# Performance work log

Hardware: AMD Instinct MI355X
Metric: run time of the kernel (lower is better)

## Reference

```python
import jax, jax.numpy as jnp
import numpy as np
from jax import lax

NB, NL, ND, NF = 32, 1024, 128, 16   # batch, max_nodes, d_model, n_func_groups
DT_RANK, NS, DCONV = 8, 2, 4         # ceil(128/16), d_state, d_conv


def setup_inputs() -> dict:
    key = jax.random.key(0)
    ks = jax.random.split(key, 16)
    s = 0.05
    x = jax.random.normal(ks[0], (NB, NL, ND), jnp.float32)
    # dense distance-weighted adjacency; scale by 1/NL so delta_p = dis @ delta stays O(1)
    dis_dense = jax.random.uniform(ks[1], (NB, NL, NL), dtype=jnp.float32) / NL
    gpt_emb = jax.random.normal(ks[2], (NB, ND), jnp.float32)
    fg_emb = jax.random.normal(ks[3], (NB, NF, ND), jnp.float32)
    A_log = jnp.log(jnp.tile(jnp.arange(1, NS + 1, dtype=jnp.float32), (ND, 1)))  # [d, n]
    return {
        "x": x, "dis_dense": dis_dense, "gpt_emb": gpt_emb, "fg_emb": fg_emb,
        "norm_w": jnp.ones((ND,), jnp.float32),
        "in_proj_w": jax.random.normal(ks[4], (2 * ND, ND), jnp.float32) * s,
        "conv_w": jax.random.normal(ks[5], (ND, 1, DCONV), jnp.float32) * s,  # depthwise OIH
        "conv_b": jax.random.normal(ks[6], (ND,), jnp.float32) * s,
        "x_proj_w": jax.random.normal(ks[7], (DT_RANK + 2 * NS, ND), jnp.float32) * s,
        "dt_proj_w": jax.random.normal(ks[8], (ND, DT_RANK), jnp.float32) * s,
        "dt_proj_b": jax.random.normal(ks[9], (ND,), jnp.float32) * s,
        "A_log": A_log,
        "D_skip": jnp.ones((ND,), jnp.float32),
        "out_proj_w": jax.random.normal(ks[10], (ND, ND), jnp.float32) * s,
        "film_w1": jax.random.normal(ks[11], (ND, ND), jnp.float32) * s,
        "film_b1": jax.random.normal(ks[12], (ND,), jnp.float32) * s,
        "film_w2": jax.random.normal(ks[13], (2 * ND, ND), jnp.float32) * s,
        "film_b2": jax.random.normal(ks[14], (2 * ND,), jnp.float32) * s,
    }


def reference(x, dis_dense, gpt_emb, fg_emb, norm_w, in_proj_w, conv_w, conv_b,
              x_proj_w, dt_proj_w, dt_proj_b, A_log, D_skip, out_proj_w,
              film_w1, film_b1, film_w2, film_b2):
    d_model = x.shape[-1]
    # RMSNorm
    x1 = x * lax.rsqrt(jnp.mean(x * x, axis=-1, keepdims=True) + 1e-5) * norm_w
    atoms = x1  # gnn treated as identity
    # CrossAttentionFusion: Q=atoms, K=V=fg_emb
    attn = jax.nn.softmax(jnp.einsum('bnd,bfd->bnf', atoms, fg_emb)
                          / jnp.sqrt(jnp.asarray(d_model, x.dtype)), axis=-1)
    h = atoms + jnp.einsum('bnf,bfd->bnd', attn, fg_emb)
    # FiLM conditioning from gpt_emb
    gb = jax.nn.silu(gpt_emb @ film_w1.T + film_b1) @ film_w2.T + film_b2
    gamma, beta = jnp.split(gb, 2, axis=-1)
    h = h * gamma[:, None, :] + beta[:, None, :]
    # in_proj -> (x, res)
    xr = h @ in_proj_w.T
    xin, res = jnp.split(xr, 2, axis=-1)
    # depthwise causal conv1d (pad d_conv-1 on the left, truncate to l)
    xc = lax.conv_general_dilated(xin.transpose(0, 2, 1), conv_w, (1,), [(DCONV - 1, 0)],
                                  dimension_numbers=('NCH', 'OIH', 'NCH'),
                                  feature_group_count=d_model) + conv_b[None, :, None]
    xs = jax.nn.silu(xc.transpose(0, 2, 1))  # [b, l, d]
    # SSM parameterization
    x_dbl = xs @ x_proj_w.T
    dt, Bm, Cm = jnp.split(x_dbl, [DT_RANK, DT_RANK + NS], axis=-1)
    delta = jax.nn.softplus(dt @ dt_proj_w.T + dt_proj_b)  # [b, l, d]
    A = -jnp.exp(A_log)  # [d, n]
    # graph-mixed delta
    delta_p = jnp.einsum('blm,bmd->bld', dis_dense, delta)
    dA = jnp.exp(jnp.einsum('bld,dn->bldn', delta_p, A))
    dBu = jnp.einsum('bld,bln,bld->bldn', delta_p, Bm, xs)
    # sequential selective scan over l
    def step(state, inp):
        a, bu, c = inp                      # [b,d,n], [b,d,n], [b,n]
        state = a * state + bu
        return state, jnp.einsum('bdn,bn->bd', state, c)
    init = jnp.zeros((x.shape[0], d_model, NS), xs.dtype)
    _, ys = lax.scan(step, init,
                     (dA.transpose(1, 0, 2, 3), dBu.transpose(1, 0, 2, 3), Cm.transpose(1, 0, 2)))
    y = ys.transpose(1, 0, 2) + xs * D_skip
    # gate + out_proj
    y = y * jax.nn.silu(res)
    out = y @ out_proj_w.T
    out = jnp.where(jnp.isfinite(out), out, jnp.zeros((), out.dtype))
    return out + x1  # residual add
```

## Files before the change

### kernel.cpp

```cpp
#include <hip/hip_runtime.h>
#include <hip/hip_bf16.h>
#include <math.h>

#define NB 32
#define NL 1024
#define ND 128
#define NF 16
#define DT_RANK 8
#define NS 2
#define DCONV 4
#define NCHUNK 32
#define CLEN 32

typedef __attribute__((ext_vector_type(8))) short bf16x8;
typedef __attribute__((ext_vector_type(4))) float f32x4;

__device__ inline unsigned short f2bf(float x) {
    unsigned u = __float_as_uint(x);
    return (unsigned short)((u + 0x7fffu + ((u >> 16) & 1u)) >> 16);
}
__device__ inline unsigned pk2(float a, float b) {
    return (unsigned)f2bf(a) | ((unsigned)f2bf(b) << 16);
}

__global__ __launch_bounds__(128)
void film_kernel(const float* __restrict__ gpt_emb,
                 const float* __restrict__ w1, const float* __restrict__ b1,
                 const float* __restrict__ w2, const float* __restrict__ b2,
                 float* __restrict__ gb)
{
    int b = blockIdx.x, t = threadIdx.x;
    __shared__ float sg[ND];
    __shared__ float sh[ND];
    sg[t] = gpt_emb[b * ND + t];
    __syncthreads();
    float a = b1[t];
    #pragma unroll 8
    for (int d = 0; d < ND; ++d) a += sg[d] * w1[t * ND + d];
    sh[t] = a / (1.f + expf(-a));
    __syncthreads();
    float g0 = b2[t], g1 = b2[ND + t];
    #pragma unroll 8
    for (int j = 0; j < ND; ++j) {
        float hv = sh[j];
        g0 += hv * w2[t * ND + j];
        g1 += hv * w2[(ND + t) * ND + j];
    }
    gb[b * 256 + t]      = g0;
    gb[b * 256 + ND + t] = g1;
}

__global__ __launch_bounds__(128)
void fused_pre_kernel(const float* __restrict__ x, const float* __restrict__ fg_emb,
                      const float* __restrict__ norm_w, const float* __restrict__ gb,
                      float* __restrict__ x1_out, float* __restrict__ h_out)
{
    int l = blockIdx.x, b = blockIdx.y, t = threadIdx.x;
    __shared__ float sh[ND];
    __shared__ float sred[2];
    __shared__ float sc[NF];
    long row = ((long)b * NL + l) * ND;
    float v = x[row + t];
    float ss = v * v;
    #pragma unroll
    for (int o = 32; o >= 1; o >>= 1) ss += __shfl_xor(ss, o);
    if ((t & 63) == 0) sred[t >> 6] = ss;
    __syncthreads();
    float mean = (sred[0] + sred[1]) * (1.f / (float)ND);
    float x1v = v * rsqrtf(mean + 1e-5f) * norm_w[t];
    sh[t] = x1v;
    __syncthreads();
    int f = t >> 3, i = t & 7;
    const float* fgb = fg_emb + ((long)b * NF + f) * ND;
    float p = 0.f;
    #pragma unroll
    for (int e = 0; e < 16; ++e) p += sh[i * 16 + e] * fgb[i * 16 + e];
    p += __shfl_xor(p, 1);
    p += __shfl_xor(p, 2);
    p += __shfl_xor(p, 4);
    if (i == 0) sc[f] = p * 0.08838834764831845f;
    __syncthreads();
    float mx = sc[0];
    #pragma unroll
    for (int ff = 1; ff < NF; ++ff) mx = fmaxf(mx, sc[ff]);
    float wv[NF];
    float wsum = 0.f;
    #pragma unroll
    for (int ff = 0; ff < NF; ++ff) { wv[ff] = expf(sc[ff] - mx); wsum += wv[ff]; }
    float inv = 1.f / wsum;
    float hv = x1v;
    #pragma unroll
    for (int ff = 0; ff < NF; ++ff)
        hv += wv[ff] * inv * fg_emb[((long)b * NF + ff) * ND + t];
    float gamma = gb[b * 256 + t];
    float beta  = gb[b * 256 + ND + t];
    hv = hv * gamma + beta;
    x1_out[row + t] = x1v;
    h_out[row + t]  = hv;
}

template <int EPI>
__global__ __launch_bounds__(256)
void wgemm_kernel(const float* __restrict__ A, const float* __restrict__ W,
                  float* __restrict__ C, const float* __restrict__ X1, int ldc)
{
    __shared__ __align__(16) unsigned short As[64 * 136];
    __shared__ __align__(16) unsigned short Ws[128 * 136];
    int m0 = blockIdx.x * 64, n0 = blockIdx.y * 128;
    int t = threadIdx.x;
    int lane = t & 63, w = t >> 6, lrow = lane & 15, lgrp = lane >> 4;
    {
        int r = t >> 2, c = t & 3;
        const float* Ap = A + ((long)(m0 + r)) * 128;
        #pragma unroll
        for (int q = 0; q < 4; ++q) {
            int col = c * 8 + q * 32;
            float4 v0 = *(const float4*)(Ap + col);
            float4 v1 = *(const float4*)(Ap + col + 4);
            int4 pv;
            pv.x = pk2(v0.x, v0.y); pv.y = pk2(v0.z, v0.w);
            pv.z = pk2(v1.x, v1.y); pv.w = pk2(v1.z, v1.w);
            *(int4*)((char*)As + r * 272 + col * 2) = pv;
        }
    }
    {
        int r = t >> 1, h2 = t & 1;
        const float* Wp = W + ((long)(n0 + r)) * 128;
        #pragma unroll
        for (int p = 0; p < 8; ++p) {
            int col = h2 * 8 + p * 16;
            float4 v0 = *(const float4*)(Wp + col);
            float4 v1 = *(const float4*)(Wp + col + 4);
            int4 pv;
            pv.x = pk2(v0.x, v0.y); pv.y = pk2(v0.z, v0.w);
            pv.z = pk2(v1.x, v1.y); pv.w = pk2(v1.z, v1.w);
            *(int4*)((char*)Ws + r * 272 + col * 2) = pv;
        }
    }
    __syncthreads();
    const char* Ar = (const char*)As + (w * 16 + lrow) * 272 + lgrp * 16;
    const char* Wr = (const char*)Ws + lrow * 272 + lgrp * 16;
    bf16x8 a[4];
    #pragma unroll
    for (int c4 = 0; c4 < 4; ++c4) a[c4] = *(const bf16x8*)(Ar + c4 * 64);
    f32x4 acc[8];
    #pragma unroll
    for (int i = 0; i < 8; ++i) acc[i] = (f32x4){0.f, 0.f, 0.f, 0.f};
    #pragma unroll
    for (int nb = 0; nb < 8; ++nb) {
        #pragma unroll
        for (int c4 = 0; c4 < 4; ++c4) {
            bf16x8 bb = *(const bf16x8*)(Wr + nb * 16 * 272 + c4 * 64);
            acc[nb] = __builtin_amdgcn_mfma_f32_16x16x32_bf16(a[c4], bb, acc[nb], 0, 0, 0);
        }
    }
    #pragma unroll
    for (int nb = 0; nb < 8; ++nb) {
        #pragma unroll
        for (int r = 0; r < 4; ++r) {
            long m = m0 + w * 16 + lgrp * 4 + r;
            int n = n0 + nb * 16 + lrow;
            float v = acc[nb][r];
            if (EPI == 1) {
                if (!isfinite(v)) v = 0.f;
                v += X1[m * ND + n];
            }
            C[m * ldc + n] = v;
        }
    }
}

__global__ __launch_bounds__(128)
void conv_xproj_kernel(const float* __restrict__ xr,
                       const float* __restrict__ conv_w, const float* __restrict__ conv_b,
                       const float* __restrict__ x_proj_w,
                       const float* __restrict__ dt_proj_w, const float* __restrict__ dt_proj_b,
                       float* __restrict__ xs_out, unsigned short* __restrict__ delta_out,
                       float* __restrict__ bc_out)
{
    int l = blockIdx.x, b = blockIdx.y, d = threadIdx.x;
    __shared__ float sxs[ND];
    __shared__ float sdbl[DT_RANK + 2 * NS];
    long base = (long)b * NL + l;
    float acc = conv_b[d];
    #pragma unroll
    for (int k = 0; k < DCONV; ++k) {
        int ll = l + k - (DCONV - 1);
        float xv = (ll >= 0) ? xr[((long)b * NL + ll) * 256 + d] : 0.f;
        acc += conv_w[d * DCONV + k] * xv;
    }
    float xsv = acc / (1.f + expf(-acc));
    sxs[d] = xsv;
    xs_out[base * ND + d] = xsv;
    __syncthreads();
    int j = d >> 3, i = d & 7;
    if (j < DT_RANK + 2 * NS) {
        const float* wrow = x_proj_w + j * ND;
        float p = 0.f;
        #pragma unroll
        for (int e = 0; e < 16; ++e) p += sxs[i * 16 + e] * wrow[i * 16 + e];
        p += __shfl_xor(p, 1);
        p += __shfl_xor(p, 2);
        p += __shfl_xor(p, 4);
        if (i == 0) sdbl[j] = p;
    }
    __syncthreads();
    float a = dt_proj_b[d];
    #pragma unroll
    for (int r = 0; r < DT_RANK; ++r) a += sdbl[r] * dt_proj_w[d * DT_RANK + r];
    float dl = (a > 20.f) ? a : log1pf(expf(a));
    delta_out[base * ND + d] = f2bf(dl);
    if (d < 4) bc_out[base * 4 + d] = sdbl[DT_RANK + d];
}

__global__ __launch_bounds__(256)
void transpose_kernel(const unsigned short* __restrict__ din,
                      unsigned short* __restrict__ dout)
{
    __shared__ __align__(16) unsigned short T[64 * 72];
    int b = blockIdx.z, d0 = blockIdx.y * 64, l0 = blockIdx.x * 64;
    int t = threadIdx.x;
    int lr = t >> 2, c = t & 3;
    const unsigned short* src = din + ((long)b * NL + l0 + lr) * ND + d0;
    #pragma unroll
    for (int j = 0; j < 2; ++j) {
        int ds_ = (c + j * 4) * 8;
        *(int4*)&T[lr * 72 + ds_] = *(const int4*)(src + ds_);
    }
    __syncthreads();
    int dr = t >> 2;
    unsigned short* dst = dout + ((long)b * ND + d0 + dr) * NL + l0;
    #pragma unroll
    for (int j = 0; j < 2; ++j) {
        int ls = (c + j * 4) * 8;
        unsigned short tmp[8];
        #pragma unroll
        for (int e = 0; e < 8; ++e) tmp[e] = T[(ls + e) * 72 + dr];
        *(int4*)(dst + ls) = *(int4*)tmp;
    }
}

__global__ __launch_bounds__(256)
void dpgemm_kernel(const float* __restrict__ dis, const unsigned short* __restrict__ dbt,
                   float* __restrict__ dp)
{
    __shared__ __align__(16) unsigned short As[64 * 72];
    __shared__ __align__(16) unsigned short Bs[128 * 72];
    int b = blockIdx.y, m0 = blockIdx.x * 64;
    int t = threadIdx.x;
    int lane = t & 63, w = t >> 6, lrow = lane & 15, lgrp = lane >> 4;
    int ar = t >> 2, ac = t & 3;
    int br = t >> 1, bh = t & 1;
    const float* Ag = dis + ((long)b * NL + m0 + ar) * NL;
    const unsigned short* Bg = dbt + ((long)b * ND + br) * NL;
    f32x4 acc[8];
    #pragma unroll
    for (int i = 0; i < 8; ++i) acc[i] = (f32x4){0.f, 0.f, 0.f, 0.f};
    const char* Ar = (const char*)As + (w * 16 + lrow) * 144 + lgrp * 16;
    const char* Br = (const char*)Bs + lrow * 144 + lgrp * 16;

    for (int k0 = 0; k0 < NL; k0 += 64) {
        #pragma unroll
        for (int q = 0; q < 4; ++q) {
            float4 v = *(const float4*)(Ag + k0 + ac * 4 + q * 16);
            unsigned long long pv = (unsigned long long)pk2(v.x, v.y)
                                  | ((unsigned long long)pk2(v.z, v.w) << 32);
            *(unsigned long long*)((char*)As + ar * 144 + ac * 8 + q * 32) = pv;
        }
        #pragma unroll
        for (int j = 0; j < 4; ++j) {
            int slot = bh * 4 + j;
            *(int4*)((char*)Bs + br * 144 + slot * 16) =
                *(const int4*)(Bg + k0 + slot * 8);
        }
        __syncthreads();
        bf16x8 a0 = *(const bf16x8*)(Ar);
        bf16x8 a1 = *(const bf16x8*)(Ar + 64);
        #pragma unroll
        for (int nb = 0; nb < 8; ++nb) {
            bf16x8 b0 = *(const bf16x8*)(Br + nb * 16 * 144);
            bf16x8 b1 = *(const bf16x8*)(Br + nb * 16 * 144 + 64);
            acc[nb] = __builtin_amdgcn_mfma_f32_16x16x32_bf16(a0, b0, acc[nb], 0, 0, 0);
            acc[nb] = __builtin_amdgcn_mfma_f32_16x16x32_bf16(a1, b1, acc[nb], 0, 0, 0);
        }
        __syncthreads();
    }
    float* Cp = dp + ((long)b * NL + m0 + w * 16 + lgrp * 4) * ND + lrow;
    #pragma unroll
    for (int nb = 0; nb < 8; ++nb)
        #pragma unroll
        for (int r = 0; r < 4; ++r)
            Cp[(long)r * ND + nb * 16] = acc[nb][r];
}

__global__ __launch_bounds__(128)
void scan_pass1(const float* __restrict__ delta_p, const float* __restrict__ xs,
                const float* __restrict__ bc, const float* __restrict__ A_log,
                float* __restrict__ Pc, float* __restrict__ Sc)
{
    int c = blockIdx.x, b = blockIdx.y, d = threadIdx.x;
    float A0 = -expf(A_log[d * NS + 0]);
    float A1 = -expf(A_log[d * NS + 1]);
    int l0 = c * CLEN;
    const float* dp_p = delta_p + ((long)b * NL + l0) * ND + d;
    const float* xs_p = xs      + ((long)b * NL + l0) * ND + d;
    const float* bc_p = bc      + ((long)b * NL + l0) * 4;
    float p0 = 1.f, p1 = 1.f, s0 = 0.f, s1 = 0.f;
    #pragma unroll 4
    for (int t = 0; t < CLEN; ++t) {
        float dp = dp_p[(long)t * ND];
        float xv = xs_p[(long)t * ND];
        float B0 = bc_p[t * 4 + 0], B1 = bc_p[t * 4 + 1];
        float a0 = expf(dp * A0), a1 = expf(dp * A1);
        float u = dp * xv;
        s0 = a0 * s0 + u * B0;
        s1 = a1 * s1 + u * B1;
        p0 *= a0;
        p1 *= a1;
    }
    long o = ((long)(b * NCHUNK + c) * 2) * ND + d;
    Pc[o] = p0; Pc[o + ND] = p1;
    Sc[o] = s0; Sc[o + ND] = s1;
}

__global__ __launch_bounds__(128)
void scan_combine(const float* __restrict__ Pc, const float* __restrict__ Sc,
                  float* __restrict__ init)
{
    int b = blockIdx.x, d = threadIdx.x;
    float s0 = 0.f, s1 = 0.f;
    #pragma unroll 4
    for (int c = 0; c < NCHUNK; ++c) {
        long o = ((long)(b * NCHUNK + c) * 2) * ND + d;
        init[o] = s0; init[o + ND] = s1;
        s0 = Pc[o] * s0 + Sc[o];
        s1 = Pc[o + ND] * s1 + Sc[o + ND];
    }
}

__global__ __launch_bounds__(128)
void scan_pass3(const float* __restrict__ delta_p, const float* __restrict__ xs,
                const float* __restrict__ bc, const float* __restrict__ xr,
                const float* __restrict__ A_log, const float* __restrict__ D_skip,
                const float* __restrict__ init, float* __restrict__ yg)
{
    int c = blockIdx.x, b = blockIdx.y, d = threadIdx.x;
    float A0 = -expf(A_log[d * NS + 0]);
    float A1 = -expf(A_log[d * NS + 1]);
    float Dd = D_skip[d];
    long o = ((long)(b * NCHUNK + c) * 2) * ND + d;
    float s0 = init[o], s1 = init[o + ND];
    int l0 = c * CLEN;
    const float* dp_p  = delta_p + ((long)b * NL + l0) * ND + d;
    const float* xs_p  = xs      + ((long)b * NL + l0) * ND + d;
    const float* bc_p  = bc      + ((long)b * NL + l0) * 4;
    const float* res_p = xr      + ((long)b * NL + l0) * 256 + ND + d;
    float* yg_p        = yg      + ((long)b * NL + l0) * ND + d;
    #pragma unroll 4
    for (int t = 0; t < CLEN; ++t) {
        float dp = dp_p[(long)t * ND];
        float xv = xs_p[(long)t * ND];
        float B0 = bc_p[t * 4 + 0], B1 = bc_p[t * 4 + 1];
        float C0 = bc_p[t * 4 + 2], C1 = bc_p[t * 4 + 3];
        float a0 = expf(dp * A0), a1 = expf(dp * A1);
        float u = dp * xv;
        s0 = a0 * s0 + u * B0;
        s1 = a1 * s1 + u * B1;
        float y = s0 * C0 + s1 * C1 + xv * Dd;
        float r = res_p[(long)t * 256];
        yg_p[(long)t * ND] = y * (r / (1.f + expf(-r)));
    }
}

extern "C" void kernel_launch(void* const* d_in, const int* in_sizes, int n_in,
                              void* d_out, int out_size, void* d_ws, size_t ws_size,
                              hipStream_t stream)
{
    const float* x         = (const float*)d_in[0];
    const float* dis       = (const float*)d_in[1];
    const float* gpt       = (const float*)d_in[2];
    const float* fg        = (const float*)d_in[3];
    const float* norm_w    = (const float*)d_in[4];
    const float* in_proj_w = (const float*)d_in[5];
    const float* conv_w    = (const float*)d_in[6];
    const float* conv_b    = (const float*)d_in[7];
    const float* x_proj_w  = (const float*)d_in[8];
    const float* dt_proj_w = (const float*)d_in[9];
    const float* dt_proj_b = (const float*)d_in[10];
    const float* A_log     = (const float*)d_in[11];
    const float* D_skip    = (const float*)d_in[12];
    const float* out_proj_w= (const float*)d_in[13];
    const float* film_w1   = (const float*)d_in[14];
    const float* film_b1   = (const float*)d_in[15];
    const float* film_w2   = (const float*)d_in[16];
    const float* film_b2   = (const float*)d_in[17];

    float* ws = (float*)d_ws;
    const size_t S = (size_t)NB * NL * ND;
    float* x1    = ws;
    float* h     = ws + S;
    float* xr    = ws + 2 * S;
    float* xs    = ws + 4 * S;
    unsigned short* delta_b = (unsigned short*)(ws + 5 * S);
    unsigned short* dbt     = delta_b + S;
    float* yg    = ws + 5 * S;
    float* bc    = ws + 6 * S;
    float* gb    = ws + 6 * S + (size_t)NB * NL * 4;
    float* scr   = gb + (size_t)NB * 256;
    const size_t CS = (size_t)NB * NCHUNK * 2 * ND;
    float* Pc    = scr;
    float* Sc    = scr + CS;
    float* initb = scr + 2 * CS;
    float* delta_p = h;

    film_kernel<<<NB, 128, 0, stream>>>(gpt, film_w1, film_b1, film_w2, film_b2, gb);

    fused_pre_kernel<<<dim3(NL, NB), 128, 0, stream>>>(x, fg, norm_w, gb, x1, h);

    wgemm_kernel<0><<<dim3(512, 2), 256, 0, stream>>>(h, in_proj_w, xr, nullptr, 256);

    conv_xproj_kernel<<<dim3(NL, NB), 128, 0, stream>>>(
        xr, conv_w, conv_b, x_proj_w, dt_proj_w, dt_proj_b, xs, delta_b, bc);

    transpose_kernel<<<dim3(16, 2, NB), 256, 0, stream>>>(delta_b, dbt);

    dpgemm_kernel<<<dim3(16, NB), 256, 0, stream>>>(dis, dbt, delta_p);

    scan_pass1<<<dim3(NCHUNK, NB), 128, 0, stream>>>(delta_p, xs, bc, A_log, Pc, Sc);
    scan_combine<<<NB, 128, 0, stream>>>(Pc, Sc, initb);
    scan_pass3<<<dim3(NCHUNK, NB), 128, 0, stream>>>(
        delta_p, xs, bc, xr, A_log, D_skip, initb, yg);

    wgemm_kernel<1><<<dim3(512, 1), 256, 0, stream>>>(yg, out_proj_w, (float*)d_out, x1, 128);
}
```

Before: 382.4 us.

## Fuse norm/attention/FiLM into in_proj GEMM and conv/xproj with delta transpose

Pre-converts the in_proj and out_proj weights to bf16 once, inside the FiLM launch. RMSNorm, cross-attention, FiLM and the in_proj MFMA GEMM now run in one 64-row tile kernel, so the fp32 h intermediate never goes to global memory. The conv, x_proj and dt_proj work is tiled over 64 rows and writes delta already transposed, which removes the separate transpose kernel. The scan writes the gated output as bf16 for a leaner out_proj GEMM that reads weights straight from global memory. This cuts launches and global memory traffic, at the cost of more LDS and registers per block and bf16 rounding of yg.

```diff
diff --git a/kernel.cpp b/kernel.cpp
--- a/kernel.cpp
+++ b/kernel.cpp
@@ -24,12 +24,29 @@
 }
 
 __global__ __launch_bounds__(128)
-void film_kernel(const float* __restrict__ gpt_emb,
-                 const float* __restrict__ w1, const float* __restrict__ b1,
-                 const float* __restrict__ w2, const float* __restrict__ b2,
-                 float* __restrict__ gb)
-{
-    int b = blockIdx.x, t = threadIdx.x;
+void film_wconv_kernel(const float* __restrict__ gpt_emb,
+                       const float* __restrict__ w1, const float* __restrict__ b1,
+                       const float* __restrict__ w2, const float* __restrict__ b2,
+                       float* __restrict__ gb,
+                       const float* __restrict__ Wi_f, const float* __restrict__ Wo_f,
+                       unsigned short* __restrict__ Wi, unsigned short* __restrict__ Wo)
+{
+    int blk = blockIdx.x, t = threadIdx.x;
+    if (blk >= NB) {
+        int i = (blk - NB) * 512 + t * 4;
+        if (i < 2 * ND * ND) {
+            float4 v = *(const float4*)&Wi_f[i];
+            int2 pv = { (int)pk2(v.x, v.y), (int)pk2(v.z, v.w) };
+            *(int2*)&Wi[i] = pv;
+        } else {
+            int j = i - 2 * ND * ND;
+            float4 v = *(const float4*)&Wo_f[j];
+            int2 pv = { (int)pk2(v.x, v.y), (int)pk2(v.z, v.w) };
+            *(int2*)&Wo[j] = pv;
+        }
+        return;
+    }
+    int b = blk;
     __shared__ float sg[ND];
     __shared__ float sh[ND];
     sg[t] = gpt_emb[b * ND + t];
@@ -50,193 +67,179 @@
     gb[b * 256 + ND + t] = g1;
 }
 
-__global__ __launch_bounds__(128)
-void fused_pre_kernel(const float* __restrict__ x, const float* __restrict__ fg_emb,
-                      const float* __restrict__ norm_w, const float* __restrict__ gb,
-                      float* __restrict__ x1_out, float* __restrict__ h_out)
-{
-    int l = blockIdx.x, b = blockIdx.y, t = threadIdx.x;
-    __shared__ float sh[ND];
-    __shared__ float sred[2];
-    __shared__ float sc[NF];
-    long row = ((long)b * NL + l) * ND;
-    float v = x[row + t];
-    float ss = v * v;
-    #pragma unroll
-    for (int o = 32; o >= 1; o >>= 1) ss += __shfl_xor(ss, o);
-    if ((t & 63) == 0) sred[t >> 6] = ss;
-    __syncthreads();
-    float mean = (sred[0] + sred[1]) * (1.f / (float)ND);
-    float x1v = v * rsqrtf(mean + 1e-5f) * norm_w[t];
-    sh[t] = x1v;
-    __syncthreads();
-    int f = t >> 3, i = t & 7;
-    const float* fgb = fg_emb + ((long)b * NF + f) * ND;
-    float p = 0.f;
-    #pragma unroll
-    for (int e = 0; e < 16; ++e) p += sh[i * 16 + e] * fgb[i * 16 + e];
-    p += __shfl_xor(p, 1);
-    p += __shfl_xor(p, 2);
-    p += __shfl_xor(p, 4);
-    if (i == 0) sc[f] = p * 0.08838834764831845f;
-    __syncthreads();
+__global__ __launch_bounds__(256)
+void pre_gemm_kernel(const float* __restrict__ x, const float* __restrict__ fg_emb,
+                     const float* __restrict__ norm_w, const float* __restrict__ gb,
+                     const unsigned short* __restrict__ Wi,
+                     float* __restrict__ x1_out, float* __restrict__ xr_out)
+{
+    __shared__ float fgs[NF * ND];
+    __shared__ float nws[ND];
+    __shared__ float gbs[2 * ND];
+    __shared__ __align__(16) unsigned short h_lds[64 * 136];
+    int b = blockIdx.y, l0 = blockIdx.x * 64;
+    int t = threadIdx.x;
+    {
+        const float* src = fg_emb + (long)b * NF * ND;
+        *(float4*)&fgs[t * 8]     = *(const float4*)&src[t * 8];
+        *(float4*)&fgs[t * 8 + 4] = *(const float4*)&src[t * 8 + 4];
+        if (t < ND) nws[t] = norm_w[t];
+        gbs[t] = gb[b * 256 + t];
+    }
+    int r = t >> 2, c = t & 3;
+    const float* xp = x + ((long)b * NL + l0 + r) * ND + c * 32;
+    float xv[32];
+    float ss = 0.f;
+    #pragma unroll
+    for (int q = 0; q < 8; ++q) {
+        float4 v = *(const float4*)(xp + q * 4);
+        xv[q * 4] = v.x; xv[q * 4 + 1] = v.y; xv[q * 4 + 2] = v.z; xv[q * 4 + 3] = v.w;
+        ss += v.x * v.x + v.y * v.y + v.z * v.z + v.w * v.w;
+    }
+    ss += __shfl_xor(ss, 1);
+    ss += __shfl_xor(ss, 2);
+    __syncthreads();
+    float rinv = rsqrtf(ss * (1.f / (float)ND) + 1e-5f);
+    #pragma unroll
+    for (int e = 0; e < 32; ++e) xv[e] = xv[e] * rinv * nws[c * 32 + e];
+    float* x1p = x1_out + ((long)b * NL + l0 + r) * ND + c * 32;
+    #pragma unroll
+    for (int q = 0; q < 8; ++q) {
+        float4 v = { xv[q * 4], xv[q * 4 + 1], xv[q * 4 + 2], xv[q * 4 + 3] };
+        *(float4*)(x1p + q * 4) = v;
+    }
+    float sc[NF];
+    #pragma unroll
+    for (int f = 0; f < NF; ++f) {
+        const float* fp = &fgs[f * ND + c * 32];
+        float p = 0.f;
+        #pragma unroll
+        for (int e = 0; e < 32; ++e) p += xv[e] * fp[e];
+        p += __shfl_xor(p, 1);
+        p += __shfl_xor(p, 2);
+        sc[f] = p * 0.08838834764831845f;
+    }
     float mx = sc[0];
     #pragma unroll
-    for (int ff = 1; ff < NF; ++ff) mx = fmaxf(mx, sc[ff]);
-    float wv[NF];
+    for (int f = 1; f < NF; ++f) mx = fmaxf(mx, sc[f]);
     float wsum = 0.f;
     #pragma unroll
-    for (int ff = 0; ff < NF; ++ff) { wv[ff] = expf(sc[ff] - mx); wsum += wv[ff]; }
+    for (int f = 0; f < NF; ++f) { sc[f] = expf(sc[f] - mx); wsum += sc[f]; }
     float inv = 1.f / wsum;
-    float hv = x1v;
-    #pragma unroll
-    for (int ff = 0; ff < NF; ++ff)
-        hv += wv[ff] * inv * fg_emb[((long)b * NF + ff) * ND + t];
-    float gamma = gb[b * 256 + t];
-    float beta  = gb[b * 256 + ND + t];
-    hv = hv * gamma + beta;
-    x1_out[row + t] = x1v;
-    h_out[row + t]  = hv;
-}
-
-template <int EPI>
+    #pragma unroll
+    for (int f = 0; f < NF; ++f) sc[f] *= inv;
+    unsigned* hrow = (unsigned*)h_lds;
+    int hbase = (r * 136 + c * 32) >> 1;
+    #pragma unroll
+    for (int e = 0; e < 32; e += 2) {
+        int d0 = c * 32 + e;
+        float h0 = xv[e], h1 = xv[e + 1];
+        #pragma unroll
+        for (int f = 0; f < NF; ++f) {
+            const float* fp = &fgs[f * ND + d0];
+            h0 += sc[f] * fp[0];
+            h1 += sc[f] * fp[1];
+        }
+        h0 = h0 * gbs[d0]     + gbs[128 + d0];
+        h1 = h1 * gbs[d0 + 1] + gbs[128 + d0 + 1];
+        hrow[hbase + (e >> 1)] = pk2(h0, h1);
+    }
+    __syncthreads();
+    int lane = t & 63, w = t >> 6, lrow = lane & 15, lgrp = lane >> 4;
+    const unsigned short* Ab = h_lds + (w * 16 + lrow) * 136 + lgrp * 8;
+    bf16x8 a[4];
+    #pragma unroll
+    for (int c4 = 0; c4 < 4; ++c4) a[c4] = *(const bf16x8*)(Ab + c4 * 32);
+    f32x4 acc[16];
+    #pragma unroll
+    for (int i = 0; i < 16; ++i) acc[i] = (f32x4){0.f, 0.f, 0.f, 0.f};
+    #pragma unroll
+    for (int nb = 0; nb < 16; ++nb) {
+        #pragma unroll
+        for (int c4 = 0; c4 < 4; ++c4) {
+            bf16x8 bb = *(const bf16x8*)(Wi + (nb * 16 + lrow) * ND + lgrp * 8 + c4 * 32);
+            acc[nb] = __builtin_amdgcn_mfma_f32_16x16x32_bf16(a[c4], bb, acc[nb], 0, 0, 0);
+        }
+    }
+    float* Cp = xr_out + ((long)b * NL + l0 + w * 16 + lgrp * 4) * 256 + lrow;
+    #pragma unroll
+    for (int nb = 0; nb < 16; ++nb)
+        #pragma unroll
+        for (int reg = 0; reg < 4; ++reg)
+            Cp[(long)reg * 256 + nb * 16] = acc[nb][reg];
+}
+
 __global__ __launch_bounds__(256)
-void wgemm_kernel(const float* __restrict__ A, const float* __restrict__ W,
-                  float* __restrict__ C, const float* __restrict__ X1, int ldc)
-{
-    __shared__ __align__(16) unsigned short As[64 * 136];
-    __shared__ __align__(16) unsigned short Ws[128 * 136];
-    int m0 = blockIdx.x * 64, n0 = blockIdx.y * 128;
-    int t = threadIdx.x;
-    int lane = t & 63, w = t >> 6, lrow = lane & 15, lgrp = lane >> 4;
-    {
-        int r = t >> 2, c = t & 3;
-        const float* Ap = A + ((long)(m0 + r)) * 128;
-        #pragma unroll
-        for (int q = 0; q < 4; ++q) {
-            int col = c * 8 + q * 32;
-            float4 v0 = *(const float4*)(Ap + col);
-            float4 v1 = *(const float4*)(Ap + col + 4);
-            int4 pv;
-            pv.x = pk2(v0.x, v0.y); pv.y = pk2(v0.z, v0.w);
-            pv.z = pk2(v1.x, v1.y); pv.w = pk2(v1.z, v1.w);
-            *(int4*)((char*)As + r * 272 + col * 2) = pv;
-        }
-    }
-    {
-        int r = t >> 1, h2 = t & 1;
-        const float* Wp = W + ((long)(n0 + r)) * 128;
-        #pragma unroll
-        for (int p = 0; p < 8; ++p) {
-            int col = h2 * 8 + p * 16;
-            float4 v0 = *(const float4*)(Wp + col);
-            float4 v1 = *(const float4*)(Wp + col + 4);
-            int4 pv;
-            pv.x = pk2(v0.x, v0.y); pv.y = pk2(v0.z, v0.w);
-            pv.z = pk2(v1.x, v1.y); pv.w = pk2(v1.z, v1.w);
-            *(int4*)((char*)Ws + r * 272 + col * 2) = pv;
-        }
-    }
-    __syncthreads();
-    const char* Ar = (const char*)As + (w * 16 + lrow) * 272 + lgrp * 16;
-    const char* Wr = (const char*)Ws + lrow * 272 + lgrp * 16;
-    bf16x8 a[4];
-    #pragma unroll
-    for (int c4 = 0; c4 < 4; ++c4) a[c4] = *(const bf16x8*)(Ar + c4 * 64);
-    f32x4 acc[8];
-    #pragma unroll
-    for (int i = 0; i < 8; ++i) acc[i] = (f32x4){0.f, 0.f, 0.f, 0.f};
-    #pragma unroll
-    for (int nb = 0; nb < 8; ++nb) {
-        #pragma unroll
-        for (int c4 = 0; c4 < 4; ++c4) {
-            bf16x8 bb = *(const bf16x8*)(Wr + nb * 16 * 272 + c4 * 64);
-            acc[nb] = __builtin_amdgcn_mfma_f32_16x16x32_bf16(a[c4], bb, acc[nb], 0, 0, 0);
-        }
-    }
-    #pragma unroll
-    for (int nb = 0; nb < 8; ++nb) {
-        #pragma unroll
-        for (int r = 0; r < 4; ++r) {
-            long m = m0 + w * 16 + lgrp * 4 + r;
-            int n = n0 + nb * 16 + lrow;
-            float v = acc[nb][r];
-            if (EPI == 1) {
-                if (!isfinite(v)) v = 0.f;
-                v += X1[m * ND + n];
-            }
-            C[m * ldc + n] = v;
-        }
-    }
-}
-
-__global__ __launch_bounds__(128)
 void conv_xproj_kernel(const float* __restrict__ xr,
                        const float* __restrict__ conv_w, const float* __restrict__ conv_b,
                        const float* __restrict__ x_proj_w,
                        const float* __restrict__ dt_proj_w, const float* __restrict__ dt_proj_b,
-                       float* __restrict__ xs_out, unsigned short* __restrict__ delta_out,
+                       float* __restrict__ xs_out, unsigned short* __restrict__ dbt,
                        float* __restrict__ bc_out)
 {
-    int l = blockIdx.x, b = blockIdx.y, d = threadIdx.x;
-    __shared__ float sxs[ND];
-    __shared__ float sdbl[DT_RANK + 2 * NS];
-    long base = (long)b * NL + l;
-    float acc = conv_b[d];
-    #pragma unroll
-    for (int k = 0; k < DCONV; ++k) {
-        int ll = l + k - (DCONV - 1);
-        float xv = (ll >= 0) ? xr[((long)b * NL + ll) * 256 + d] : 0.f;
-        acc += conv_w[d * DCONV + k] * xv;
-    }
-    float xsv = acc / (1.f + expf(-acc));
-    sxs[d] = xsv;
-    xs_out[base * ND + d] = xsv;
-    __syncthreads();
-    int j = d >> 3, i = d & 7;
-    if (j < DT_RANK + 2 * NS) {
-        const float* wrow = x_proj_w + j * ND;
-        float p = 0.f;
-        #pragma unroll
-        for (int e = 0; e < 16; ++e) p += sxs[i * 16 + e] * wrow[i * 16 + e];
-        p += __shfl_xor(p, 1);
-        p += __shfl_xor(p, 2);
-        p += __shfl_xor(p, 4);
-        if (i == 0) sdbl[j] = p;
-    }
-    __syncthreads();
-    float a = dt_proj_b[d];
-    #pragma unroll
-    for (int r = 0; r < DT_RANK; ++r) a += sdbl[r] * dt_proj_w[d * DT_RANK + r];
-    float dl = (a > 20.f) ? a : log1pf(expf(a));
-    delta_out[base * ND + d] = f2bf(dl);
-    if (d < 4) bc_out[base * 4 + d] = sdbl[DT_RANK + d];
-}
-
-__global__ __launch_bounds__(256)
-void transpose_kernel(const unsigned short* __restrict__ din,
-                      unsigned short* __restrict__ dout)
-{
-    __shared__ __align__(16) unsigned short T[64 * 72];
-    int b = blockIdx.z, d0 = blockIdx.y * 64, l0 = blockIdx.x * 64;
+    __shared__ float xin[67 * 132];
+    __shared__ float xsl[64 * 129];
+    unsigned short* T = (unsigned short*)xin;
+    int b = blockIdx.y, l0 = blockIdx.x * 64;
     int t = threadIdx.x;
-    int lr = t >> 2, c = t & 3;
-    const unsigned short* src = din + ((long)b * NL + l0 + lr) * ND + d0;
-    #pragma unroll
-    for (int j = 0; j < 2; ++j) {
-        int ds_ = (c + j * 4) * 8;
-        *(int4*)&T[lr * 72 + ds_] = *(const int4*)(src + ds_);
-    }
-    __syncthreads();
-    int dr = t >> 2;
-    unsigned short* dst = dout + ((long)b * ND + d0 + dr) * NL + l0;
-    #pragma unroll
-    for (int j = 0; j < 2; ++j) {
-        int ls = (c + j * 4) * 8;
-        unsigned short tmp[8];
-        #pragma unroll
-        for (int e = 0; e < 8; ++e) tmp[e] = T[(ls + e) * 72 + dr];
-        *(int4*)(dst + ls) = *(int4*)tmp;
+    for (int i = t; i < 67 * 32; i += 256) {
+        int rr = i >> 5, c4 = i & 31;
+        int l = l0 - 3 + rr;
+        float4 v = {0.f, 0.f, 0.f, 0.f};
+        if (l >= 0) v = *(const float4*)(xr + ((long)b * NL + l) * 256 + c4 * 4);
+        *(float4*)&xin[rr * 132 + c4 * 4] = v;
+    }
+    __syncthreads();
+    {
+        int d = t & 127, rg = t >> 7;
+        float w0 = conv_w[d * 4], w1 = conv_w[d * 4 + 1];
+        float w2 = conv_w[d * 4 + 2], w3 = conv_w[d * 4 + 3];
+        float cb = conv_b[d];
+        for (int r = rg; r < 64; r += 2) {
+            float acc = cb + w0 * xin[r * 132 + d] + w1 * xin[(r + 1) * 132 + d]
+                           + w2 * xin[(r + 2) * 132 + d] + w3 * xin[(r + 3) * 132 + d];
+            float xsv = acc / (1.f + expf(-acc));
+            xsl[r * 129 + d] = xsv;
+            xs_out[((long)b * NL + l0 + r) * ND + d] = xsv;
+        }
+    }
+    __syncthreads();
+    {
+        int r = t >> 2, c = t & 3;
+        float dbl[12];
+        #pragma unroll
+        for (int j = 0; j < 12; ++j) {
+            const float* wr = x_proj_w + j * ND + c * 32;
+            const float* xp = &xsl[r * 129 + c * 32];
+            float p = 0.f;
+            #pragma unroll
+            for (int e = 0; e < 32; ++e) p += xp[e] * wr[e];
+            p += __shfl_xor(p, 1);
+            p += __shfl_xor(p, 2);
+            dbl[j] = p;
+        }
+        if (c == 0) {
+            float4 v = { dbl[8], dbl[9], dbl[10], dbl[11] };
+            *(float4*)(bc_out + ((long)b * NL + l0 + r) * 4) = v;
+        }
+        #pragma unroll
+        for (int e = 0; e < 32; ++e) {
+            int d = c * 32 + e;
+            float a = dt_proj_b[d];
+            #pragma unroll
+            for (int q = 0; q < DT_RANK; ++q) a += dbl[q] * dt_proj_w[d * DT_RANK + q];
+            float dl = (a > 20.f) ? a : log1pf(expf(a));
+            T[d * 72 + r] = f2bf(dl);
+        }
+    }
+    __syncthreads();
+    {
+        int dr = t >> 1, half = t & 1;
+        unsigned short* dst = dbt + ((long)b * ND + dr) * NL + l0 + half * 32;
+        const unsigned short* src = &T[dr * 72 + half * 32];
+        #pragma unroll
+        for (int q = 0; q < 4; ++q)
+            *(int4*)(dst + q * 8) = *(const int4*)(src + q * 8);
     }
 }
 
@@ -342,7 +345,7 @@
 void scan_pass3(const float* __restrict__ delta_p, const float* __restrict__ xs,
                 const float* __restrict__ bc, const float* __restrict__ xr,
                 const float* __restrict__ A_log, const float* __restrict__ D_skip,
-                const float* __restrict__ init, float* __restrict__ yg)
+                const float* __restrict__ init, unsigned short* __restrict__ yg)
 {
     int c = blockIdx.x, b = blockIdx.y, d = threadIdx.x;
     float A0 = -expf(A_log[d * NS + 0]);
@@ -355,7 +358,7 @@
     const float* xs_p  = xs      + ((long)b * NL + l0) * ND + d;
     const float* bc_p  = bc      + ((long)b * NL + l0) * 4;
     const float* res_p = xr      + ((long)b * NL + l0) * 256 + ND + d;
-    float* yg_p        = yg      + ((long)b * NL + l0) * ND + d;
+    unsigned short* yg_p = yg    + ((long)b * NL + l0) * ND + d;
     #pragma unroll 4
     for (int t = 0; t < CLEN; ++t) {
         float dp = dp_p[(long)t * ND];
@@ -368,7 +371,42 @@
         s1 = a1 * s1 + u * B1;
         float y = s0 * C0 + s1 * C1 + xv * Dd;
         float r = res_p[(long)t * 256];
-        yg_p[(long)t * ND] = y * (r / (1.f + expf(-r)));
+        yg_p[(long)t * ND] = f2bf(y * (r / (1.f + expf(-r))));
+    }
+}
+
+__global__ __launch_bounds__(256)
+void outgemm_kernel(const unsigned short* __restrict__ yg,
+                    const unsigned short* __restrict__ Wo,
+                    const float* __restrict__ X1, float* __restrict__ out)
+{
+    int m0 = blockIdx.x * 64;
+    int t = threadIdx.x, lane = t & 63, w = t >> 6, lrow = lane & 15, lgrp = lane >> 4;
+    const unsigned short* Ap = yg + ((long)(m0 + w * 16 + lrow)) * ND + lgrp * 8;
+    bf16x8 a[4];
+    #pragma unroll
+    for (int c4 = 0; c4 < 4; ++c4) a[c4] = *(const bf16x8*)(Ap + c4 * 32);
+    f32x4 acc[8];
+    #pragma unroll
+    for (int i = 0; i < 8; ++i) acc[i] = (f32x4){0.f, 0.f, 0.f, 0.f};
+    #pragma unroll
+    for (int nb = 0; nb < 8; ++nb) {
+        #pragma unroll
+        for (int c4 = 0; c4 < 4; ++c4) {
+            bf16x8 bb = *(const bf16x8*)(Wo + (nb * 16 + lrow) * ND + lgrp * 8 + c4 * 32);
+            acc[nb] = __builtin_amdgcn_mfma_f32_16x16x32_bf16(a[c4], bb, acc[nb], 0, 0, 0);
+        }
+    }
+    #pragma unroll
+    for (int nb = 0; nb < 8; ++nb) {
+        #pragma unroll
+        for (int reg = 0; reg < 4; ++reg) {
+            long m = m0 + w * 16 + lgrp * 4 + reg;
+            int n = nb * 16 + lrow;
+            float v = acc[nb][reg];
+            if (!isfinite(v)) v = 0.f;
+            out[m * ND + n] = v + X1[m * ND + n];
+        }
     }
 }
 
@@ -397,32 +435,29 @@
 
     float* ws = (float*)d_ws;
     const size_t S = (size_t)NB * NL * ND;
-    float* x1    = ws;
-    float* h     = ws + S;
-    float* xr    = ws + 2 * S;
-    float* xs    = ws + 4 * S;
-    unsigned short* delta_b = (unsigned short*)(ws + 5 * S);
-    unsigned short* dbt     = delta_b + S;
-    float* yg    = ws + 5 * S;
-    float* bc    = ws + 6 * S;
-    float* gb    = ws + 6 * S + (size_t)NB * NL * 4;
-    float* scr   = gb + (size_t)NB * 256;
+    float* x1      = ws;
+    float* xr      = ws + S;
+    float* xs      = ws + 3 * S;
+    unsigned short* dbt = (unsigned short*)(ws + 4 * S);
+    float* delta_p = ws + 4 * S + S / 2;
+    unsigned short* yg = (unsigned short*)(ws + 5 * S + S / 2);
+    float* bc      = ws + 6 * S;
+    float* gb      = bc + (size_t)NB * NL * 4;
+    unsigned short* Wi = (unsigned short*)(gb + (size_t)NB * 256);
+    unsigned short* Wo = Wi + 2 * ND * ND;
+    float* Pc      = (float*)(Wo + ND * ND);
     const size_t CS = (size_t)NB * NCHUNK * 2 * ND;
-    float* Pc    = scr;
-    float* Sc    = scr + CS;
-    float* initb = scr + 2 * CS;
-    float* delta_p = h;
-
-    film_kernel<<<NB, 128, 0, stream>>>(gpt, film_w1, film_b1, film_w2, film_b2, gb);
-
-    fused_pre_kernel<<<dim3(NL, NB), 128, 0, stream>>>(x, fg, norm_w, gb, x1, h);
-
-    wgemm_kernel<0><<<dim3(512, 2), 256, 0, stream>>>(h, in_proj_w, xr, nullptr, 256);
-
-    conv_xproj_kernel<<<dim3(NL, NB), 128, 0, stream>>>(
-        xr, conv_w, conv_b, x_proj_w, dt_proj_w, dt_proj_b, xs, delta_b, bc);
-
-    transpose_kernel<<<dim3(16, 2, NB), 256, 0, stream>>>(delta_b, dbt);
+    float* Sc      = Pc + CS;
+    float* initb   = Pc + 2 * CS;
+
+    film_wconv_kernel<<<NB + 96, 128, 0, stream>>>(
+        gpt, film_w1, film_b1, film_w2, film_b2, gb, in_proj_w, out_proj_w, Wi, Wo);
+
+    pre_gemm_kernel<<<dim3(NL / 64, NB), 256, 0, stream>>>(
+        x, fg, norm_w, gb, Wi, x1, xr);
+
+    conv_xproj_kernel<<<dim3(NL / 64, NB), 256, 0, stream>>>(
+        xr, conv_w, conv_b, x_proj_w, dt_proj_w, dt_proj_b, xs, dbt, bc);
 
     dpgemm_kernel<<<dim3(16, NB), 256, 0, stream>>>(dis, dbt, delta_p);
 
@@ -431,5 +466,5 @@
     scan_pass3<<<dim3(NCHUNK, NB), 128, 0, stream>>>(
         delta_p, xs, bc, xr, A_log, D_skip, initb, yg);
 
-    wgemm_kernel<1><<<dim3(512, 1), 256, 0, stream>>>(yg, out_proj_w, (float*)d_out, x1, 128);
-}
+    outgemm_kernel<<<512, 256, 0, stream>>>(yg, Wo, x1, (float*)d_out);
+}
```

Measured after the change: 449.5 us. 1.18x slower.
